# Performance work log

Hardware: AMD Instinct MI355X
Metric: run time of the kernel (lower is better)

The kernel has to match this reference:

```python
import jax, jax.numpy as jnp
import numpy as np

B, C, H, W = 8, 256, 64, 64
HEADS, H_SP, W_SP = 8, 64, 4  # idx=0: H_sp=resolution[0], W_sp=split_size
D = C // HEADS
SCALE = D ** -0.5
HH, WW = H // H_SP, W // W_SP  # 1, 16 (no padding needed)


def setup_inputs() -> dict:
    key = jax.random.key(0)
    k1, k2, k3 = jax.random.split(key, 3)
    temp = jax.random.normal(k1, (B, 3, C, H, W), dtype=jnp.float32)
    get_v_weight = jax.random.normal(k2, (C, 1, 3, 3), dtype=jnp.float32) * 0.1
    get_v_bias = jax.random.normal(k3, (C,), dtype=jnp.float32) * 0.1
    return {"temp": temp, "get_v_weight": get_v_weight, "get_v_bias": get_v_bias}


def _im2win_shuffle(x):
    # x: (B, C, H, W); H split as (H_SP, HH) with H_SP OUTER (shuffled windows)
    x = x.reshape(B, HEADS, D, H_SP, HH, W_SP, WW)
    x = x.transpose(0, 4, 6, 1, 3, 5, 2)  # b hh ww h H_sp W_sp d
    return x.reshape(B * HH * WW, HEADS, H_SP * W_SP, D)


def reference(temp, get_v_weight, get_v_bias):
    # H, W are multiples of H_SP, W_SP -> pad is zero (faithful to F.pad path)
    q, k, v = temp[:, 0], temp[:, 1], temp[:, 2]
    qw = _im2win_shuffle(q) * SCALE
    kw = _im2win_shuffle(k)
    vw = _im2win_shuffle(v)

    # LePE: depthwise 3x3 conv applied per shuffled window
    vimg = v.reshape(B, C, H_SP, HH, W_SP, WW).transpose(0, 3, 5, 1, 2, 4)
    vimg = vimg.reshape(B * HH * WW, C, H_SP, W_SP)
    lepe = jax.lax.conv_general_dilated(
        vimg, get_v_weight, (1, 1), ((1, 1), (1, 1)),
        dimension_numbers=("NCHW", "OIHW", "NCHW"), feature_group_count=C,
    ) + get_v_bias[None, :, None, None]
    lepe = lepe.reshape(B * HH * WW, HEADS, D, H_SP * W_SP).transpose(0, 1, 3, 2)

    attn = jax.nn.softmax(jnp.einsum("whqd,whkd->whqk", qw, kw), axis=-1)
    x = jnp.einsum("whqk,whkd->whqd", attn, vw) + lepe  # (nW, h, S, d)

    # windows2img_shuffle -> (B, C, H, W), then raw .view to (B, H, W, C)
    x = x.reshape(B, HH, WW, HEADS, H_SP, W_SP, D)
    x = x.transpose(0, 3, 6, 4, 1, 5, 2).reshape(B, C, H, W)
    x = x.reshape(B, H, W, C)  # raw memory view, matches torch .view
    return x.reshape(B, H * W, C)
```

## Files before the change

### kernel.cpp

```cpp
#include <hip/hip_runtime.h>


typedef __attribute__((ext_vector_type(8))) short bf16x8;
typedef __attribute__((ext_vector_type(4))) float floatx4;
typedef unsigned short ushort_t;
typedef unsigned int uint_t;

constexpr float QSCALE = 0.25503486f;
constexpr size_t WS_NEED = 3ull * 1024 * 8192 * 2;

__device__ __forceinline__ ushort_t f2bf(float f) {
    union { float f; uint_t u; } v; v.f = f;
    uint_t r = v.u + 0x7fffu + ((v.u >> 16) & 1u);
    return (ushort_t)(r >> 16);
}
__device__ __forceinline__ float bf2f(ushort_t h) {
    union { uint_t u; float f; } v; v.u = ((uint_t)h) << 16;
    return v.f;
}

__global__ __launch_bounds__(256, 8)
void pack_kernel(const float* __restrict__ temp, ushort_t* __restrict__ ws)
{
    const int bi = blockIdx.x;
    const int b = bi / 384;
    const int rem = bi % 384;
    const int m = rem >> 7;
    const int hd = (rem >> 4) & 7;
    const int slab = rem & 15;

    __shared__ ushort_t Lb[4 * 2182];

    const int u = threadIdx.x;
    const float4* src4 = (const float4*)(temp + ((size_t)((b * 3 + m) * 256 + hd * 32)) * 4096);

    #pragma unroll
    for (int i = 0; i < 8; i++) {
        const int flat = i * 256 + u;
        const int w4 = flat & 15, h = (flat >> 4) & 3, d = flat >> 6;
        float4 v = src4[(size_t)d * 1024 + slab * 64 + h * 16 + w4];
        if (m == 0) { v.x *= QSCALE; v.y *= QSCALE; v.z *= QSCALE; v.w *= QSCALE; }
        const int base = h * 2182 + (w4 * 4) * 34 + d;
        Lb[base]       = f2bf(v.x);
        Lb[base + 34]  = f2bf(v.y);
        Lb[base + 68]  = f2bf(v.z);
        Lb[base + 102] = f2bf(v.w);
    }
    __syncthreads();

    const int t0 = slab * 16;
    if (m < 2) {
        #pragma unroll
        for (int i = 0; i < 4; i++) {
            const int c2 = i * 256 + u;
            const int dc = c2 & 3, tl = (c2 >> 2) & 15, ww = c2 >> 6;
            const int h = tl >> 2, w = (tl & 3) * 16 + ww;
            const uint_t* lp = (const uint_t*)&Lb[h * 2182 + w * 34 + dc * 8];
            uint4 val; val.x = lp[0]; val.y = lp[1]; val.z = lp[2]; val.w = lp[3];
            const size_t prob = (size_t)((b * 8 + hd) * 16 + ww);
            *(uint4*)(ws + prob * 16384 + (size_t)m * 8192 + (t0 + tl) * 32 + dc * 8) = val;
        }
    } else {
        #pragma unroll
        for (int i = 0; i < 2; i++) {
            const int c2 = i * 256 + u;
            const int d = c2 & 31, ww = (c2 >> 5) & 15;
            union { ushort_t us[16]; uint4 q[2]; } vv;
            #pragma unroll
            for (int tl = 0; tl < 16; tl++)
                vv.us[tl] = Lb[(tl >> 2) * 2182 + ((tl & 3) * 16 + ww) * 34 + d];
            const size_t prob = (size_t)((b * 8 + hd) * 16 + ww);
            uint4* dst = (uint4*)(ws + 16777216ull + prob * 8192 + d * 256 + t0);
            dst[0] = vv.q[0]; dst[1] = vv.q[1];
        }
    }
}

template<bool PACKED>
__global__ __launch_bounds__(256, 4)
void attn_kernel(const float* __restrict__ temp, ushort_t* __restrict__ ws,
                 const float* __restrict__ wgt, const float* __restrict__ bias,
                 float* __restrict__ out)
{
    const int B_ = blockIdx.x;
    const int bh = B_ & 63, ww = B_ >> 6;
    const int hd = bh & 7, b = bh >> 3;
    const int plin = bh * 16 + ww;

    __shared__ ushort_t Ks[256 * 40];
    __shared__ ushort_t Vt[32 * 264];

    const int u = threadIdx.x;
    const int wv = u >> 6, ln = u & 63;
    const int lm = ln & 15, q4 = ln >> 4, l7 = ln & 7, b8 = (ln >> 3) & 1;

    const int pa_w0 = (wv * 64 + b8 * 16 + q4 * 4) * 40 + 32 + l7;
    const int pa_w1 = (wv * 64 + (2 + b8) * 16 + q4 * 4) * 40 + 32 + l7;
    const int pa_rd = (wv * 64 + ln) * 40 + 32;

    bf16x8 qa[4];

    if (PACKED) {
        const size_t pb = (size_t)plin * 16384;
        {
            const uint4* s = (const uint4*)(ws + pb + 8192 + u * 32);
            uint4* d = (uint4*)&Ks[u * 40];
            d[0] = s[0]; d[1] = s[1]; d[2] = s[2]; d[3] = s[3];
        }
        {
            const int dd = u >> 3, seg = u & 7;
            const uint4* s = (const uint4*)(ws + 16777216ull + (size_t)plin * 8192 + dd * 256 + seg * 32);
            uint4* d = (uint4*)&Vt[dd * 264 + seg * 32];
            d[0] = s[0]; d[1] = s[1]; d[2] = s[2]; d[3] = s[3];
        }
        #pragma unroll
        for (int T = 0; T < 4; T++) {
            const int Tg = wv * 4 + T;
            qa[T] = *(const bf16x8*)(ws + pb + (Tg * 16 + lm) * 32 + q4 * 8);
        }
    } else {
        const float* qp = temp + ((size_t)(b * 3 + 0) * 256 + hd * 32) * 4096 + ww;
        const float* kp = temp + ((size_t)(b * 3 + 1) * 256 + hd * 32) * 4096 + ww;
        const float* vp = temp + ((size_t)(b * 3 + 2) * 256 + hd * 32) * 4096 + ww;
        {
            union { ushort_t us[32]; uint4 q[4]; } tmp;
            #pragma unroll
            for (int d = 0; d < 32; d++) tmp.us[d] = f2bf(kp[(size_t)d * 4096 + u * 16]);
            uint4* dst = (uint4*)&Ks[u * 40];
            dst[0] = tmp.q[0]; dst[1] = tmp.q[1]; dst[2] = tmp.q[2]; dst[3] = tmp.q[3];
        }
        #pragma unroll
        for (int d = 0; d < 32; d++) Vt[d * 264 + u] = f2bf(vp[(size_t)d * 4096 + u * 16]);
        #pragma unroll
        for (int T = 0; T < 4; T++) {
            const int Tg = wv * 4 + T, q = Tg * 16 + lm;
            union { ushort_t us[8]; bf16x8 v; } f;
            #pragma unroll
            for (int j = 0; j < 8; j++)
                f.us[j] = f2bf(qp[(size_t)(q4 * 8 + j) * 4096 + q * 16] * QSCALE);
            qa[T] = f.v;
        }
    }
    __syncthreads();

    floatx4 acc[4][2];
    float lrow[4][4];
    #pragma unroll
    for (int T = 0; T < 4; T++) {
        acc[T][0] = (floatx4)0.0f; acc[T][1] = (floatx4)0.0f;
        #pragma unroll
        for (int r = 0; r < 4; r++) lrow[T][r] = 0.0f;
    }

    for (int c = 0; c < 8; c++) {
        const bf16x8 kb0 = *(const bf16x8*)&Ks[(c * 32 + lm) * 40 + q4 * 8];
        const bf16x8 kb1 = *(const bf16x8*)&Ks[(c * 32 + 16 + lm) * 40 + q4 * 8];
        const bf16x8 vb0 = *(const bf16x8*)&Vt[lm * 264 + c * 32 + q4 * 8];
        const bf16x8 vb1 = *(const bf16x8*)&Vt[(16 + lm) * 264 + c * 32 + q4 * 8];
        #pragma unroll
        for (int T = 0; T < 4; T++) {
            floatx4 s0 = __builtin_amdgcn_mfma_f32_16x16x32_bf16(qa[T], kb0, (floatx4)0.0f, 0, 0, 0);
            floatx4 s1 = __builtin_amdgcn_mfma_f32_16x16x32_bf16(qa[T], kb1, (floatx4)0.0f, 0, 0, 0);
            #pragma unroll
            for (int r = 0; r < 4; r++) {
                const float p0 = exp2f(s0[r]);
                const float p1 = exp2f(s1[r]);
                const ushort_t h0 = f2bf(p0), h1 = f2bf(p1);
                lrow[T][r] += bf2f(h0) + bf2f(h1);
                Ks[pa_w0 + r * 40] = h0;
                Ks[pa_w1 + r * 40] = h1;
            }
            const bf16x8 pa = *(const bf16x8*)&Ks[pa_rd];
            acc[T][0] = __builtin_amdgcn_mfma_f32_16x16x32_bf16(pa, vb0, acc[T][0], 0, 0, 0);
            acc[T][1] = __builtin_amdgcn_mfma_f32_16x16x32_bf16(pa, vb1, acc[T][1], 0, 0, 0);
        }
    }

    float wc[2][9], bs[2];
    #pragma unroll
    for (int dt = 0; dt < 2; dt++) {
        const int d = dt * 16 + lm;
        #pragma unroll
        for (int k = 0; k < 9; k++) wc[dt][k] = wgt[(hd * 32 + d) * 9 + k];
        bs[dt] = bias[hd * 32 + d];
    }

    float* Of = (float*)ws + (size_t)plin * 8192;
    float* ob = out + ((size_t)b * 256 + hd * 32) * 4096 + ww;

    #pragma unroll
    for (int T = 0; T < 4; T++) {
        const int Tg = wv * 4 + T;
        const int hs = Tg * 4 + q4;
        float inv[4];
        #pragma unroll
        for (int r = 0; r < 4; r++) {
            float ls = lrow[T][r];
            ls += __shfl_xor(ls, 1); ls += __shfl_xor(ls, 2);
            ls += __shfl_xor(ls, 4); ls += __shfl_xor(ls, 8);
            inv[r] = 1.0f / ls;
        }
        #pragma unroll
        for (int dt = 0; dt < 2; dt++) {
            const int d = dt * 16 + lm;
            float vv[3][4];
            #pragma unroll
            for (int dy = 0; dy < 3; dy++) {
                const int hh = hs + dy - 1;
                if (hh >= 0 && hh < 64) {
                    #pragma unroll
                    for (int cx = 0; cx < 4; cx++) vv[dy][cx] = bf2f(Vt[d * 264 + hh * 4 + cx]);
                } else {
                    #pragma unroll
                    for (int cx = 0; cx < 4; cx++) vv[dy][cx] = 0.0f;
                }
            }
            #pragma unroll
            for (int r = 0; r < 4; r++) {
                float lep = bs[dt];
                #pragma unroll
                for (int dy = 0; dy < 3; dy++) {
                    #pragma unroll
                    for (int kx = 0; kx < 3; kx++) {
                        const int wsrc = r + kx - 1;
                        if (wsrc >= 0 && wsrc < 4) lep += wc[dt][dy * 3 + kx] * vv[dy][wsrc];
                    }
                }
                const int q = Tg * 16 + q4 * 4 + r;
                const float val = acc[T][dt][r] * inv[r] + lep;
                if (PACKED) Of[q * 32 + d] = val;
                else        ob[(size_t)d * 4096 + q * 16] = val;
            }
        }
    }
}

__global__ __launch_bounds__(256, 4)
void scatter_kernel(const float* __restrict__ Of, float* __restrict__ out)
{
    const int bi = blockIdx.x;
    const int b = bi >> 7, hd = (bi >> 4) & 7, slab = bi & 15;
    const int bh = b * 8 + hd;
    const int t0 = slab * 16;

    __shared__ float T2[16 * 545];

    const int u = threadIdx.x;

    #pragma unroll
    for (int i = 0; i < 8; i++) {
        const int f = i * 256 + u;
        const int d4 = f & 7, t = (f >> 3) & 15, ww = f >> 7;
        const float4 v = ((const float4*)Of)[(size_t)(bh * 16 + ww) * 2048 + (t0 + t) * 8 + d4];
        const int base = t * 545 + (d4 * 4) * 17 + ww;
        T2[base]      = v.x;
        T2[base + 17] = v.y;
        T2[base + 34] = v.z;
        T2[base + 51] = v.w;
    }
    __syncthreads();

    float4* out4 = (float4*)(out + ((size_t)b * 256 + hd * 32) * 4096);
    #pragma unroll
    for (int i = 0; i < 8; i++) {
        const int g = i * 256 + u;
        const int ww4 = g & 3, t = (g >> 2) & 15, d = g >> 6;
        const int base = t * 545 + d * 17 + ww4 * 4;
        float4 v;
        v.x = T2[base]; v.y = T2[base + 1]; v.z = T2[base + 2]; v.w = T2[base + 3];
        out4[(size_t)d * 1024 + (t0 + t) * 4 + ww4] = v;
    }
}

extern "C" void kernel_launch(void* const* d_in, const int* in_sizes, int n_in,
                              void* d_out, int out_size, void* d_ws, size_t ws_size,
                              hipStream_t stream) {
    const float* temp = (const float*)d_in[0];
    const float* wgt  = (const float*)d_in[1];
    const float* bias = (const float*)d_in[2];
    float* out = (float*)d_out;

    if (ws_size >= WS_NEED) {
        ushort_t* ws = (ushort_t*)d_ws;
        pack_kernel<<<dim3(3072), dim3(256), 0, stream>>>(temp, ws);
        attn_kernel<true><<<dim3(1024), dim3(256), 0, stream>>>(temp, ws, wgt, bias, out);
        scatter_kernel<<<dim3(1024), dim3(256), 0, stream>>>((const float*)d_ws, out);
    } else {
        attn_kernel<false><<<dim3(1024), dim3(256), 0, stream>>>(temp, (ushort_t*)d_ws, wgt, bias, out);
    }
}
```

Before: 214.2 us.

## Fuse pack, attention and scatter into one kernel processing four windows per block

Replaces the three-kernel pipeline (global-memory bf16 repack, attention, scatter transpose) with a single kernel. Each 1024-thread block handles four adjacent shuffled windows so that float4 loads of the input and float4 stores of the output are coalesced across the window index. Q, K and V are converted and laid out in shared memory, and the output is transposed through shared memory as well. This removes the workspace round trips and two kernel launches. In exchange it uses about 146KB of LDS per block and launches only 256 blocks, which limits occupancy and latency hiding.

```diff
diff --git a/kernel.cpp b/kernel.cpp
--- a/kernel.cpp
+++ b/kernel.cpp
@@ -7,7 +7,6 @@
 typedef unsigned int uint_t;
 
 constexpr float QSCALE = 0.25503486f;
-constexpr size_t WS_NEED = 3ull * 1024 * 8192 * 2;
 
 __device__ __forceinline__ ushort_t f2bf(float f) {
     union { float f; uint_t u; } v; v.f = f;
@@ -19,129 +18,90 @@
     return v.f;
 }
 
-__global__ __launch_bounds__(256, 8)
-void pack_kernel(const float* __restrict__ temp, ushort_t* __restrict__ ws)
+constexpr int KSP = 10240;
+constexpr int VTB = 4 * KSP;
+constexpr int VTP = 8448;
+constexpr int OBP = 8704;
+
+__global__ __launch_bounds__(1024, 4)
+void fused_kernel(const float* __restrict__ temp, const float* __restrict__ wgt,
+                  const float* __restrict__ bias, float* __restrict__ out)
 {
-    const int bi = blockIdx.x;
-    const int b = bi / 384;
-    const int rem = bi % 384;
-    const int m = rem >> 7;
-    const int hd = (rem >> 4) & 7;
-    const int slab = rem & 15;
-
-    __shared__ ushort_t Lb[4 * 2182];
+    const int bid = blockIdx.x;
+    const int hd = bid & 7, b = (bid >> 3) & 7, wwg = bid >> 6;
+
+    __shared__ __align__(16) ushort_t SM[74752];
 
     const int u = threadIdx.x;
-    const float4* src4 = (const float4*)(temp + ((size_t)((b * 3 + m) * 256 + hd * 32)) * 4096);
-
-    #pragma unroll
-    for (int i = 0; i < 8; i++) {
-        const int flat = i * 256 + u;
-        const int w4 = flat & 15, h = (flat >> 4) & 3, d = flat >> 6;
-        float4 v = src4[(size_t)d * 1024 + slab * 64 + h * 16 + w4];
-        if (m == 0) { v.x *= QSCALE; v.y *= QSCALE; v.z *= QSCALE; v.w *= QSCALE; }
-        const int base = h * 2182 + (w4 * 4) * 34 + d;
-        Lb[base]       = f2bf(v.x);
-        Lb[base + 34]  = f2bf(v.y);
-        Lb[base + 68]  = f2bf(v.z);
-        Lb[base + 102] = f2bf(v.w);
-    }
-    __syncthreads();
-
-    const int t0 = slab * 16;
-    if (m < 2) {
-        #pragma unroll
-        for (int i = 0; i < 4; i++) {
-            const int c2 = i * 256 + u;
-            const int dc = c2 & 3, tl = (c2 >> 2) & 15, ww = c2 >> 6;
-            const int h = tl >> 2, w = (tl & 3) * 16 + ww;
-            const uint_t* lp = (const uint_t*)&Lb[h * 2182 + w * 34 + dc * 8];
-            uint4 val; val.x = lp[0]; val.y = lp[1]; val.z = lp[2]; val.w = lp[3];
-            const size_t prob = (size_t)((b * 8 + hd) * 16 + ww);
-            *(uint4*)(ws + prob * 16384 + (size_t)m * 8192 + (t0 + tl) * 32 + dc * 8) = val;
-        }
-    } else {
-        #pragma unroll
-        for (int i = 0; i < 2; i++) {
-            const int c2 = i * 256 + u;
-            const int d = c2 & 31, ww = (c2 >> 5) & 15;
-            union { ushort_t us[16]; uint4 q[2]; } vv;
-            #pragma unroll
-            for (int tl = 0; tl < 16; tl++)
-                vv.us[tl] = Lb[(tl >> 2) * 2182 + ((tl & 3) * 16 + ww) * 34 + d];
-            const size_t prob = (size_t)((b * 8 + hd) * 16 + ww);
-            uint4* dst = (uint4*)(ws + 16777216ull + prob * 8192 + d * 256 + t0);
-            dst[0] = vv.q[0]; dst[1] = vv.q[1];
-        }
-    }
-}
-
-template<bool PACKED>
-__global__ __launch_bounds__(256, 4)
-void attn_kernel(const float* __restrict__ temp, ushort_t* __restrict__ ws,
-                 const float* __restrict__ wgt, const float* __restrict__ bias,
-                 float* __restrict__ out)
-{
-    const int B_ = blockIdx.x;
-    const int bh = B_ & 63, ww = B_ >> 6;
-    const int hd = bh & 7, b = bh >> 3;
-    const int plin = bh * 16 + ww;
-
-    __shared__ ushort_t Ks[256 * 40];
-    __shared__ ushort_t Vt[32 * 264];
-
-    const int u = threadIdx.x;
-    const int wv = u >> 6, ln = u & 63;
+    const int g = u >> 6, p = g >> 2, wv = g & 3;
+    const int ln = u & 63;
     const int lm = ln & 15, q4 = ln >> 4, l7 = ln & 7, b8 = (ln >> 3) & 1;
 
-    const int pa_w0 = (wv * 64 + b8 * 16 + q4 * 4) * 40 + 32 + l7;
-    const int pa_w1 = (wv * 64 + (2 + b8) * 16 + q4 * 4) * 40 + 32 + l7;
-    const int pa_rd = (wv * 64 + ln) * 40 + 32;
+    const float4* Tq = (const float4*)temp + (((size_t)(b * 3) * 256 + hd * 32) * 1024 + wwg);
+    const float4* Tk = Tq + (size_t)256 * 1024;
+    const float4* Tv = Tk + (size_t)256 * 1024;
+
+    union F4 { float4 v; float a[4]; };
+
+    #pragma unroll
+    for (int i = 0; i < 4; i++) {
+        const int flat = i * 1024 + u;
+        const int d2 = flat & 15, t = flat >> 4;
+        const int d = d2 * 2;
+        F4 v0, v1;
+        v0.v = Tq[(size_t)d * 1024 + t * 4];
+        v1.v = Tq[(size_t)(d + 1) * 1024 + t * 4];
+        #pragma unroll
+        for (int pp = 0; pp < 4; pp++) {
+            const uint_t pk = (uint_t)f2bf(v0.a[pp] * QSCALE)
+                            | ((uint_t)f2bf(v1.a[pp] * QSCALE) << 16);
+            *(uint_t*)&SM[pp * KSP + t * 40 + d] = pk;
+        }
+    }
+    __syncthreads();
 
     bf16x8 qa[4];
-
-    if (PACKED) {
-        const size_t pb = (size_t)plin * 16384;
-        {
-            const uint4* s = (const uint4*)(ws + pb + 8192 + u * 32);
-            uint4* d = (uint4*)&Ks[u * 40];
-            d[0] = s[0]; d[1] = s[1]; d[2] = s[2]; d[3] = s[3];
-        }
-        {
-            const int dd = u >> 3, seg = u & 7;
-            const uint4* s = (const uint4*)(ws + 16777216ull + (size_t)plin * 8192 + dd * 256 + seg * 32);
-            uint4* d = (uint4*)&Vt[dd * 264 + seg * 32];
-            d[0] = s[0]; d[1] = s[1]; d[2] = s[2]; d[3] = s[3];
-        }
-        #pragma unroll
-        for (int T = 0; T < 4; T++) {
-            const int Tg = wv * 4 + T;
-            qa[T] = *(const bf16x8*)(ws + pb + (Tg * 16 + lm) * 32 + q4 * 8);
-        }
-    } else {
-        const float* qp = temp + ((size_t)(b * 3 + 0) * 256 + hd * 32) * 4096 + ww;
-        const float* kp = temp + ((size_t)(b * 3 + 1) * 256 + hd * 32) * 4096 + ww;
-        const float* vp = temp + ((size_t)(b * 3 + 2) * 256 + hd * 32) * 4096 + ww;
-        {
-            union { ushort_t us[32]; uint4 q[4]; } tmp;
-            #pragma unroll
-            for (int d = 0; d < 32; d++) tmp.us[d] = f2bf(kp[(size_t)d * 4096 + u * 16]);
-            uint4* dst = (uint4*)&Ks[u * 40];
-            dst[0] = tmp.q[0]; dst[1] = tmp.q[1]; dst[2] = tmp.q[2]; dst[3] = tmp.q[3];
-        }
-        #pragma unroll
-        for (int d = 0; d < 32; d++) Vt[d * 264 + u] = f2bf(vp[(size_t)d * 4096 + u * 16]);
-        #pragma unroll
-        for (int T = 0; T < 4; T++) {
-            const int Tg = wv * 4 + T, q = Tg * 16 + lm;
-            union { ushort_t us[8]; bf16x8 v; } f;
-            #pragma unroll
-            for (int j = 0; j < 8; j++)
-                f.us[j] = f2bf(qp[(size_t)(q4 * 8 + j) * 4096 + q * 16] * QSCALE);
-            qa[T] = f.v;
-        }
-    }
-    __syncthreads();
+    #pragma unroll
+    for (int T = 0; T < 4; T++) {
+        const int Tg = wv * 4 + T;
+        qa[T] = *(const bf16x8*)&SM[p * KSP + (Tg * 16 + lm) * 40 + q4 * 8];
+    }
+    __syncthreads();
+
+    #pragma unroll
+    for (int i = 0; i < 4; i++) {
+        const int flat = i * 1024 + u;
+        const int d2 = flat & 15, t = flat >> 4;
+        const int d = d2 * 2;
+        F4 v0, v1;
+        v0.v = Tk[(size_t)d * 1024 + t * 4];
+        v1.v = Tk[(size_t)(d + 1) * 1024 + t * 4];
+        #pragma unroll
+        for (int pp = 0; pp < 4; pp++) {
+            const uint_t pk = (uint_t)f2bf(v0.a[pp]) | ((uint_t)f2bf(v1.a[pp]) << 16);
+            *(uint_t*)&SM[pp * KSP + t * 40 + d] = pk;
+        }
+    }
+    #pragma unroll
+    for (int i = 0; i < 4; i++) {
+        const int flat = i * 1024 + u;
+        const int t2 = flat & 127, d = flat >> 7;
+        F4 va, vb;
+        va.v = Tv[(size_t)d * 1024 + t2 * 8];
+        vb.v = Tv[(size_t)d * 1024 + t2 * 8 + 4];
+        #pragma unroll
+        for (int pp = 0; pp < 4; pp++) {
+            const uint_t pk = (uint_t)f2bf(va.a[pp]) | ((uint_t)f2bf(vb.a[pp]) << 16);
+            *(uint_t*)&SM[VTB + pp * VTP + d * 264 + t2 * 2] = pk;
+        }
+    }
+    __syncthreads();
+
+    const int pK = p * KSP;
+    const int pV = VTB + p * VTP;
+    const int pa_w0 = pK + (wv * 64 + b8 * 16 + q4 * 4) * 40 + 32 + l7;
+    const int pa_w1 = pK + (wv * 64 + (2 + b8) * 16 + q4 * 4) * 40 + 32 + l7;
+    const int pa_rd = pK + (wv * 64 + ln) * 40 + 32;
 
     floatx4 acc[4][2];
     float lrow[4][4];
@@ -153,10 +113,10 @@
     }
 
     for (int c = 0; c < 8; c++) {
-        const bf16x8 kb0 = *(const bf16x8*)&Ks[(c * 32 + lm) * 40 + q4 * 8];
-        const bf16x8 kb1 = *(const bf16x8*)&Ks[(c * 32 + 16 + lm) * 40 + q4 * 8];
-        const bf16x8 vb0 = *(const bf16x8*)&Vt[lm * 264 + c * 32 + q4 * 8];
-        const bf16x8 vb1 = *(const bf16x8*)&Vt[(16 + lm) * 264 + c * 32 + q4 * 8];
+        const bf16x8 kb0 = *(const bf16x8*)&SM[pK + (c * 32 + lm) * 40 + q4 * 8];
+        const bf16x8 kb1 = *(const bf16x8*)&SM[pK + (c * 32 + 16 + lm) * 40 + q4 * 8];
+        const bf16x8 vb0 = *(const bf16x8*)&SM[pV + lm * 264 + c * 32 + q4 * 8];
+        const bf16x8 vb1 = *(const bf16x8*)&SM[pV + (16 + lm) * 264 + c * 32 + q4 * 8];
         #pragma unroll
         for (int T = 0; T < 4; T++) {
             floatx4 s0 = __builtin_amdgcn_mfma_f32_16x16x32_bf16(qa[T], kb0, (floatx4)0.0f, 0, 0, 0);
@@ -167,26 +127,23 @@
                 const float p1 = exp2f(s1[r]);
                 const ushort_t h0 = f2bf(p0), h1 = f2bf(p1);
                 lrow[T][r] += bf2f(h0) + bf2f(h1);
-                Ks[pa_w0 + r * 40] = h0;
-                Ks[pa_w1 + r * 40] = h1;
-            }
-            const bf16x8 pa = *(const bf16x8*)&Ks[pa_rd];
+                SM[pa_w0 + r * 40] = h0;
+                SM[pa_w1 + r * 40] = h1;
+            }
+            const bf16x8 pa = *(const bf16x8*)&SM[pa_rd];
             acc[T][0] = __builtin_amdgcn_mfma_f32_16x16x32_bf16(pa, vb0, acc[T][0], 0, 0, 0);
             acc[T][1] = __builtin_amdgcn_mfma_f32_16x16x32_bf16(pa, vb1, acc[T][1], 0, 0, 0);
         }
     }
 
-    float wc[2][9], bs[2];
+    float wc[2][9], bs2[2];
     #pragma unroll
     for (int dt = 0; dt < 2; dt++) {
         const int d = dt * 16 + lm;
         #pragma unroll
         for (int k = 0; k < 9; k++) wc[dt][k] = wgt[(hd * 32 + d) * 9 + k];
-        bs[dt] = bias[hd * 32 + d];
-    }
-
-    float* Of = (float*)ws + (size_t)plin * 8192;
-    float* ob = out + ((size_t)b * 256 + hd * 32) * 4096 + ww;
+        bs2[dt] = bias[hd * 32 + d];
+    }
 
     #pragma unroll
     for (int T = 0; T < 4; T++) {
@@ -209,7 +166,7 @@
                 const int hh = hs + dy - 1;
                 if (hh >= 0 && hh < 64) {
                     #pragma unroll
-                    for (int cx = 0; cx < 4; cx++) vv[dy][cx] = bf2f(Vt[d * 264 + hh * 4 + cx]);
+                    for (int cx = 0; cx < 4; cx++) vv[dy][cx] = bf2f(SM[pV + d * 264 + hh * 4 + cx]);
                 } else {
                     #pragma unroll
                     for (int cx = 0; cx < 4; cx++) vv[dy][cx] = 0.0f;
@@ -217,7 +174,7 @@
             }
             #pragma unroll
             for (int r = 0; r < 4; r++) {
-                float lep = bs[dt];
+                float lep = bs2[dt];
                 #pragma unroll
                 for (int dy = 0; dy < 3; dy++) {
                     #pragma unroll
@@ -226,49 +183,39 @@
                         if (wsrc >= 0 && wsrc < 4) lep += wc[dt][dy * 3 + kx] * vv[dy][wsrc];
                     }
                 }
+                acc[T][dt][r] = acc[T][dt][r] * inv[r] + lep;
+            }
+        }
+    }
+    __syncthreads();
+
+    float* Ob = (float*)SM;
+    #pragma unroll
+    for (int T = 0; T < 4; T++) {
+        const int Tg = wv * 4 + T;
+        #pragma unroll
+        for (int dt = 0; dt < 2; dt++) {
+            const int d = dt * 16 + lm;
+            #pragma unroll
+            for (int r = 0; r < 4; r++) {
                 const int q = Tg * 16 + q4 * 4 + r;
-                const float val = acc[T][dt][r] * inv[r] + lep;
-                if (PACKED) Of[q * 32 + d] = val;
-                else        ob[(size_t)d * 4096 + q * 16] = val;
-            }
-        }
-    }
-}
-
-__global__ __launch_bounds__(256, 4)
-void scatter_kernel(const float* __restrict__ Of, float* __restrict__ out)
-{
-    const int bi = blockIdx.x;
-    const int b = bi >> 7, hd = (bi >> 4) & 7, slab = bi & 15;
-    const int bh = b * 8 + hd;
-    const int t0 = slab * 16;
-
-    __shared__ float T2[16 * 545];
-
-    const int u = threadIdx.x;
-
+                Ob[p * OBP + q * 34 + d] = acc[T][dt][r];
+            }
+        }
+    }
+    __syncthreads();
+
+    float4* out4 = (float4*)out + (((size_t)(b * 256) + hd * 32) * 1024 + wwg);
     #pragma unroll
     for (int i = 0; i < 8; i++) {
-        const int f = i * 256 + u;
-        const int d4 = f & 7, t = (f >> 3) & 15, ww = f >> 7;
-        const float4 v = ((const float4*)Of)[(size_t)(bh * 16 + ww) * 2048 + (t0 + t) * 8 + d4];
-        const int base = t * 545 + (d4 * 4) * 17 + ww;
-        T2[base]      = v.x;
-        T2[base + 17] = v.y;
-        T2[base + 34] = v.z;
-        T2[base + 51] = v.w;
-    }
-    __syncthreads();
-
-    float4* out4 = (float4*)(out + ((size_t)b * 256 + hd * 32) * 4096);
-    #pragma unroll
-    for (int i = 0; i < 8; i++) {
-        const int g = i * 256 + u;
-        const int ww4 = g & 3, t = (g >> 2) & 15, d = g >> 6;
-        const int base = t * 545 + d * 17 + ww4 * 4;
-        float4 v;
-        v.x = T2[base]; v.y = T2[base + 1]; v.z = T2[base + 2]; v.w = T2[base + 3];
-        out4[(size_t)d * 1024 + (t0 + t) * 4 + ww4] = v;
+        const int flat = i * 1024 + u;
+        const int d = flat & 31, t = flat >> 5;
+        float4 o;
+        o.x = Ob[0 * OBP + t * 34 + d];
+        o.y = Ob[1 * OBP + t * 34 + d];
+        o.z = Ob[2 * OBP + t * 34 + d];
+        o.w = Ob[3 * OBP + t * 34 + d];
+        out4[(size_t)d * 1024 + t * 4] = o;
     }
 }
 
@@ -279,13 +226,6 @@
     const float* wgt  = (const float*)d_in[1];
     const float* bias = (const float*)d_in[2];
     float* out = (float*)d_out;
-
-    if (ws_size >= WS_NEED) {
-        ushort_t* ws = (ushort_t*)d_ws;
-        pack_kernel<<<dim3(3072), dim3(256), 0, stream>>>(temp, ws);
-        attn_kernel<true><<<dim3(1024), dim3(256), 0, stream>>>(temp, ws, wgt, bias, out);
-        scatter_kernel<<<dim3(1024), dim3(256), 0, stream>>>((const float*)d_ws, out);
-    } else {
-        attn_kernel<false><<<dim3(1024), dim3(256), 0, stream>>>(temp, (ushort_t*)d_ws, wgt, bias, out);
-    }
-}
+    (void)d_ws; (void)ws_size;
+    fused_kernel<<<dim3(256), dim3(1024), 0, stream>>>(temp, wgt, bias, out);
+}
```

Result: faster. 202.7 us (-5.3%).
